# Kernel optimization log

Hardware: AMD Instinct MI355X
Metric: run time of the kernel (lower is better)

The kernel has to match this reference:

```python
import jax, jax.numpy as jnp
import numpy as np

B, C, RES, WS, HEADS, GROUPS, MLP_DIM = 16, 256, 56, 7, 8, 16, 1024
HEAD_DIM = C // HEADS
N = WS * WS  # tokens per window


def _rel_index(ws):
    coords = np.stack(np.meshgrid(np.arange(ws), np.arange(ws), indexing='ij'), 0).reshape(2, -1)
    rel = (coords[:, :, None] - coords[:, None, :]).transpose(1, 2, 0) + ws - 1
    return jnp.asarray(rel[..., 0] * (2 * ws - 1) + rel[..., 1], jnp.int32)


def setup_inputs() -> dict:
    key = jax.random.key(0)
    ks = jax.random.split(key, 8)
    s = 0.02
    return {
        'x': jax.random.normal(ks[0], (B, C, RES, RES), jnp.float32),
        'qkv_w': jax.random.normal(ks[1], (3 * C, C), jnp.float32) * s,
        'qkv_b': jnp.zeros((3 * C,), jnp.float32),
        'logit_scale': jnp.full((HEADS,), np.log(10.0), jnp.float32),
        'bias_table': jax.random.normal(ks[2], ((2 * WS - 1) ** 2, HEADS), jnp.float32) * s,
        'rel_index': _rel_index(WS),
        'proj_w': jax.random.normal(ks[3], (C, C), jnp.float32) * s,
        'proj_b': jnp.zeros((C,), jnp.float32),
        'gn1_w': jnp.ones((C,), jnp.float32), 'gn1_b': jnp.zeros((C,), jnp.float32),
        'gn2_w': jnp.ones((C,), jnp.float32), 'gn2_b': jnp.zeros((C,), jnp.float32),
        'mlp_gn_w': jnp.ones((C,), jnp.float32), 'mlp_gn_b': jnp.zeros((C,), jnp.float32),
        'mlp_w1': jax.random.normal(ks[4], (MLP_DIM, C), jnp.float32) * s,
        'mlp_b1': jnp.zeros((MLP_DIM,), jnp.float32),
        'mlp_w2': jax.random.normal(ks[5], (C, MLP_DIM), jnp.float32) * s,
        'mlp_b2': jnp.zeros((C,), jnp.float32),
    }


def _group_norm(x, w, b, groups, eps=1e-5):
    bn, c, h, ww = x.shape
    xg = x.reshape(bn, groups, c // groups, h, ww)
    m = xg.mean((2, 3, 4), keepdims=True)
    v = xg.var((2, 3, 4), keepdims=True)
    xg = (xg - m) * jax.lax.rsqrt(v + eps)
    return xg.reshape(bn, c, h, ww) * w[None, :, None, None] + b[None, :, None, None]


def _window_cosine_attn(x, qkv_w, qkv_b, logit_scale, bias_table, rel_index, proj_w, proj_b):
    bn, c, hh, ww = x.shape
    nh, nw = hh // WS, ww // WS
    # partition into non-overlapping WSxWS windows -> [bn*nh*nw, N, C]
    xw = x.reshape(bn, c, nh, WS, nw, WS).transpose(0, 2, 4, 3, 5, 1).reshape(bn * nh * nw, N, c)
    qkv = xw @ qkv_w.T + qkv_b
    qkv = qkv.reshape(-1, N, 3, HEADS, HEAD_DIM).transpose(2, 0, 3, 1, 4)
    q, k, v = qkv[0], qkv[1], qkv[2]  # [Bw, heads, N, d]
    # cosine attention (Swin v2): l2-normalized q/k, learnable clamped logit scale
    qn = q / jnp.clip(jnp.linalg.norm(q, axis=-1, keepdims=True), 1e-12)
    kn = k / jnp.clip(jnp.linalg.norm(k, axis=-1, keepdims=True), 1e-12)
    scale = jnp.exp(jnp.minimum(logit_scale, jnp.log(100.0)))[None, :, None, None]
    attn = jnp.einsum('bhnd,bhmd->bhnm', qn, kn) * scale
    bias = bias_table[rel_index].transpose(2, 0, 1)  # [heads, N, N]
    attn = jax.nn.softmax(attn + bias[None], axis=-1)
    out = jnp.einsum('bhnm,bhmd->bhnd', attn, v)
    out = out.transpose(0, 2, 1, 3).reshape(-1, N, c) @ proj_w.T + proj_b
    # reverse window partition -> [bn, c, H, W]
    out = out.reshape(bn, nh, nw, WS, WS, c).transpose(0, 5, 1, 3, 2, 4).reshape(bn, c, hh, ww)
    return out


def reference(x, qkv_w, qkv_b, logit_scale, bias_table, rel_index, proj_w, proj_b,
              gn1_w, gn1_b, gn2_w, gn2_b, mlp_gn_w, mlp_gn_b, mlp_w1, mlp_b1, mlp_w2, mlp_b2):
    h = _window_cosine_attn(x, qkv_w, qkv_b, logit_scale, bias_table, rel_index, proj_w, proj_b)
    h = jax.nn.relu(_group_norm(x + h, gn1_w, gn1_b, GROUPS))
    # ConvMLP: GroupNorm -> 1x1 conv -> act -> 1x1 conv
    m = _group_norm(h, mlp_gn_w, mlp_gn_b, GROUPS)
    m = jax.nn.relu(jnp.einsum('bchw,ec->behw', m, mlp_w1) + mlp_b1[None, :, None, None])
    m = jnp.einsum('behw,ce->bchw', m, mlp_w2) + mlp_b2[None, :, None, None]
    z = jax.nn.relu(_group_norm(h + m, gn2_w, gn2_b, GROUPS))
    return z
```

## Files before the change

kernel.cpp:

```cpp
#include <hip/hip_runtime.h>
#include <hip/hip_bf16.h>

typedef unsigned short u16;
typedef u16 u16x8 __attribute__((ext_vector_type(8)));
typedef u16 u16x4 __attribute__((ext_vector_type(4)));
typedef __bf16 bf16x8 __attribute__((ext_vector_type(8)));
typedef float f32x4 __attribute__((ext_vector_type(4)));

#define B_      16
#define C_      256
#define RES_    56
#define HW_     3136
#define NTOK    49
#define HEADS_  8
#define HD_     32
#define GROUPS_ 16
#define MLPD    1024
#define M_TOT   50176

__device__ __forceinline__ float b2f(u16 u){
  unsigned int x = ((unsigned int)u) << 16;
  return __builtin_bit_cast(float, x);
}
__device__ __forceinline__ u16 f2b(float f){
  __hip_bfloat16 h = __float2bfloat16(f);
  return __builtin_bit_cast(u16, h);
}
__device__ __forceinline__ bool sniff_f32(const void* sniff){
  return ((const u16*)sniff)[0] != (u16)0x3F80;
}
__device__ __forceinline__ float ldf(const void* p, size_t i, bool f32){
  return f32 ? ((const float*)p)[i] : b2f(((const u16*)p)[i]);
}
__device__ __forceinline__ void load8(const void* p, size_t off, bool f32, float* v){
  if (f32){
    const float* s = (const float*)p + off;
    float4 a = *(const float4*)s, b = *(const float4*)(s + 4);
    v[0]=a.x; v[1]=a.y; v[2]=a.z; v[3]=a.w; v[4]=b.x; v[5]=b.y; v[6]=b.z; v[7]=b.w;
  } else {
    u16x8 u = *(const u16x8*)((const u16*)p + off);
    #pragma unroll
    for (int j=0;j<8;++j) v[j] = b2f(u[j]);
  }
}

__device__ __forceinline__ void gload16(const u16* g, u16* l){
  __builtin_amdgcn_global_load_lds(
      (const __attribute__((address_space(1))) unsigned int*)g,
      (__attribute__((address_space(3))) unsigned int*)l, 16, 0, 0);
}

__device__ __forceinline__ int tok_of(int base_hw, int i){
  int ic = i < 48 ? i : 48;
  int q = (ic*37) >> 8;
  return base_hw + q*RES_ + (ic - q*7);
}

enum { M_QKV=0, M_PROJ=1, M_MLP1=2, M_MLP2=3 };

template<int MODE>
__global__ __launch_bounds__(256)
void mgemm(const u16* __restrict__ A, const u16* __restrict__ Bseg,
           const void* __restrict__ bias, void* __restrict__ Cp,
           const void* __restrict__ resid, float2* __restrict__ partE,
           const void* __restrict__ sniff)
{
  constexpr int KK  = (MODE==M_MLP2) ? 1024 : 256;
  constexpr bool STATS = (MODE==M_PROJ || MODE==M_MLP2);
  constexpr int BM  = STATS ? 64 : 128;
  constexpr int MFR = BM/32;
  const int nx  = gridDim.x;
  const int bid = blockIdx.y * nx + blockIdx.x;
  const int cpx = (nx * gridDim.y) >> 3;
  const int swz = (bid & 7) * cpx + (bid >> 3);
  const int n0 = (swz % nx) * 128;
  const int m0 = (swz / nx) * BM;

  __shared__ alignas(16) u16 As[BM*64];
  __shared__ alignas(16) u16 Bs[128*64];
  const int tid  = threadIdx.x;
  const int lane = tid & 63, w = tid >> 6;
  const int wm = w >> 1, wn = w & 1;
  const int lr = lane & 15, lk = lane >> 4;

  const int grow = lane >> 3, gcolg = (lane & 7) ^ (lane >> 3);
  size_t aoff[MFR], boff[4];
  #pragma unroll
  for (int i=0;i<MFR;++i){
    const int row = w*(BM/4) + i*8 + grow;
    aoff[i] = (size_t)(m0 + row)*KK + gcolg*8;
  }
  #pragma unroll
  for (int i=0;i<4;++i){
    const int row = w*32 + i*8 + grow;
    boff[i] = (size_t)(n0 + row)*KK + gcolg*8;
  }

  f32x4 acc[MFR][4];
  #pragma unroll
  for (int i=0;i<MFR;++i)
    #pragma unroll
    for (int j=0;j<4;++j) acc[i][j] = (f32x4){0.f,0.f,0.f,0.f};

  for (int k0 = 0; k0 < KK; k0 += 64){
    if (k0) __syncthreads();
    #pragma unroll
    for (int i=0;i<MFR;++i)
      gload16(A + aoff[i] + k0, As + (w*MFR+i)*512);
    #pragma unroll
    for (int i=0;i<4;++i)
      gload16(Bseg + boff[i] + k0, Bs + (w*4+i)*512);
    __syncthreads();
    #pragma unroll
    for (int kh=0; kh<2; ++kh){
      bf16x8 af[MFR], bfr[4];
      #pragma unroll
      for (int mf=0;mf<MFR;++mf){
        int row = wm*(BM/2) + mf*16 + lr;
        int idx = (row*64 + (kh*4 + lk)*8) ^ ((row&7)*8);
        af[mf] = *(const bf16x8*)(As + idx);
      }
      #pragma unroll
      for (int nf=0;nf<4;++nf){
        int row = wn*64 + nf*16 + lr;
        int idx = (row*64 + (kh*4 + lk)*8) ^ ((row&7)*8);
        bfr[nf] = *(const bf16x8*)(Bs + idx);
      }
      #pragma unroll
      for (int mf=0;mf<MFR;++mf)
        #pragma unroll
        for (int nf=0;nf<4;++nf)
          acc[mf][nf] = __builtin_amdgcn_mfma_f32_16x16x32_bf16(af[mf], bfr[nf], acc[mf][nf], 0,0,0);
    }
  }

  const bool f32 = sniff_f32(sniff);
  float bv[4];
  #pragma unroll
  for (int nf=0;nf<4;++nf)
    bv[nf] = ldf(bias, (size_t)(n0 + wn*64 + nf*16 + lr), f32);

  float sv[4] = {0.f,0.f,0.f,0.f};
  float qv[4] = {0.f,0.f,0.f,0.f};

  #pragma unroll
  for (int mf=0;mf<MFR;++mf){
    #pragma unroll
    for (int r=0;r<4;++r){
      const int row = m0 + wm*(BM/2) + mf*16 + lk*4 + r;
      #pragma unroll
      for (int nf=0;nf<4;++nf){
        const int col = n0 + wn*64 + nf*16 + lr;
        float v = acc[mf][nf][r] + bv[nf];
        if (MODE == M_QKV){
          ((u16*)Cp)[(size_t)row*768 + col] = f2b(v);
        } else if (MODE == M_MLP1){
          ((u16*)Cp)[(size_t)row*MLPD + col] = f2b(fmaxf(v, 0.f));
        } else {
          v += b2f(((const u16*)resid)[(size_t)row*C_ + col]);
          ((u16*)Cp)[(size_t)row*C_ + col] = f2b(v);
          if constexpr (STATS){ sv[nf] += v; qv[nf] += v*v; }
        }
      }
    }
  }

  if constexpr (STATS){
    const size_t tileId = (size_t)((m0>>6)*2 + (n0>>7));
    #pragma unroll
    for (int nf=0;nf<4;++nf){
      float s = sv[nf], q = qv[nf];
      #pragma unroll
      for (int m=1;m<64;m<<=1){ s += __shfl_xor(s,m); q += __shfl_xor(q,m); }
      if (lane == 0)
        partE[tileId*16 + w*4 + nf] = make_float2(s,q);
    }
  }
}

__global__ __launch_bounds__(256)
void xt_kernel(const void* __restrict__ x, u16* __restrict__ xbf,
               const void* __restrict__ sniff){
  const bool f32 = sniff_f32(sniff);
  const int hw0 = blockIdx.x*64, c0 = blockIdx.y*64, b = blockIdx.z;
  __shared__ float tile[64][65];
  const int t = threadIdx.x;
  {
    int r = t >> 2, p = t & 3;
    size_t src = ((size_t)(b*C_ + c0 + r))*HW_ + hw0 + p*16;
    float v[16];
    load8(x, src, f32, v);
    load8(x, src + 8, f32, v + 8);
    #pragma unroll
    for (int e=0;e<16;++e) tile[p*16+e][r] = v[e];
  }
  __syncthreads();
  {
    int r2 = t >> 2, p2 = t & 3;
    u16x8 o0, o1;
    #pragma unroll
    for (int e=0;e<8;++e){ o0[e] = f2b(tile[r2][p2*16+e]); o1[e] = f2b(tile[r2][p2*16+8+e]); }
    size_t dst = ((size_t)(b*HW_ + hw0 + r2))*C_ + c0 + p2*16;
    *(u16x8*)(xbf + dst)     = o0;
    *(u16x8*)(xbf + dst + 8) = o1;
  }
}

__global__ __launch_bounds__(256)
void wprep(const void* __restrict__ qkv_w, const void* __restrict__ proj_w,
           const void* __restrict__ w1, const void* __restrict__ w2,
           u16* __restrict__ wq, u16* __restrict__ wp,
           u16* __restrict__ w1b, u16* __restrict__ w2b,
           const void* __restrict__ bias_table, const int* __restrict__ rel_index,
           float* __restrict__ biasD, float* __restrict__ biasRM,
           const void* __restrict__ sniff){
  const bool f32 = sniff_f32(sniff);
  const int blk = blockIdx.x;
  if (blk < 384){
    const void* src; u16* dst; int base;
    if (blk < 96)      { src = qkv_w;  dst = wq;  base = blk; }
    else if (blk <128) { src = proj_w; dst = wp;  base = blk - 96; }
    else if (blk <256) { src = w1;     dst = w1b; base = blk - 128; }
    else               { src = w2;     dst = w2b; base = blk - 256; }
    int i = (base*256 + threadIdx.x)*8;
    float v[8];
    load8(src, (size_t)i, f32, v);
    u16x8 u;
    #pragma unroll
    for (int j=0;j<8;++j) u[j] = f2b(v[j]);
    *(u16x8*)(dst + i) = u;
  } else {
    int h = blk - 384;
    for (int idx = threadIdx.x; idx < NTOK*NTOK; idx += 256)
      biasD[h*NTOK*NTOK + idx] = ldf(bias_table, (size_t)rel_index[idx]*HEADS_ + h, f32);
    __syncthreads();
    for (int i = threadIdx.x; i < NTOK; i += 256){
      const float* row = biasD + (h*NTOK + i)*NTOK;
      float m = row[0];
      for (int j=1;j<NTOK;++j) m = fmaxf(m, row[j]);
      biasRM[h*NTOK + i] = m;
    }
  }
}

__global__ __launch_bounds__(256)
void attn_kernel(const u16* __restrict__ qkv, u16* __restrict__ attnout,
                 const void* __restrict__ logit_scale, const float* __restrict__ biasD,
                 const float* __restrict__ biasRM, const void* __restrict__ sniff)
{
  const bool f32 = sniff_f32(sniff);
  const int h = blockIdx.x & 7, w = blockIdx.x >> 3;
  const int b = w >> 6, wr = (w >> 3) & 7, wc = w & 7;
  const int tid = threadIdx.x;
  const int wv = tid >> 6, lane = tid & 63;
  const int lr = lane & 15, lg = lane >> 4;
  const int base_hw = (wr*7)*RES_ + wc*7;
  const size_t qbase = (size_t)b*HW_*768;

  __shared__ alignas(16) u16 Qn[64][40];
  __shared__ alignas(16) u16 Kn[64][40];
  __shared__ alignas(16) u16 Vt[32][72];
  __shared__ alignas(16) u16 Pl[64][72];

  const float scale = __expf(fminf(ldf(logit_scale, h, f32), 4.6051701860f));

  if (wv == 0){
    u16 vrow[32];
    if (lane < NTOK){
      const u16* src = qkv + qbase + (size_t)tok_of(base_hw, lane)*768 + 512 + h*HD_;
      u16x8 a0 = *(const u16x8*)(src), a1 = *(const u16x8*)(src+8);
      u16x8 a2 = *(const u16x8*)(src+16), a3 = *(const u16x8*)(src+24);
      #pragma unroll
      for (int e=0;e<8;++e){ vrow[e]=a0[e]; vrow[8+e]=a1[e]; vrow[16+e]=a2[e]; vrow[24+e]=a3[e]; }
    } else {
      #pragma unroll
      for (int e=0;e<32;++e) vrow[e] = 0;
    }
    #pragma unroll
    for (int d=0;d<32;++d) Vt[d][lane] = vrow[d];
  } else if (wv == 1 || wv == 2){
    float fv[32];
    if (lane < NTOK){
      const u16* src = qkv + qbase + (size_t)tok_of(base_hw, lane)*768
                     + (wv == 2 ? 0 : 256) + h*HD_;
      #pragma unroll
      for (int c8=0;c8<4;++c8){
        u16x8 u = *(const u16x8*)(src + c8*8);
        #pragma unroll
        for (int e=0;e<8;++e) fv[c8*8+e] = b2f(u[e]);
      }
    } else {
      #pragma unroll
      for (int e=0;e<32;++e) fv[e] = 0.f;
    }
    float ss = 0.f;
    #pragma unroll
    for (int d=0;d<32;++d) ss += fv[d]*fv[d];
    float inv = (wv == 2 ? scale : 1.f) / fmaxf(sqrtf(ss), 1e-12f);
    u16* dst = (wv == 2) ? &Qn[lane][0] : &Kn[lane][0];
    #pragma unroll
    for (int c8=0;c8<4;++c8){
      u16x8 u;
      #pragma unroll
      for (int e=0;e<8;++e) u[e] = f2b(fv[c8*8+e]*inv);
      *(u16x8*)(dst + c8*8) = u;
    }
  }
  __syncthreads();

  const int mt = wv;
  const int i0 = mt*16;

  bf16x8 af = *(const bf16x8*)&Qn[i0 + lr][lg*8];
  f32x4 s[4];
  #pragma unroll
  for (int nt=0;nt<4;++nt){
    bf16x8 bq = *(const bf16x8*)&Kn[nt*16 + lr][lg*8];
    f32x4 c;
    #pragma unroll
    for (int r=0;r<4;++r){
      int i = i0 + lg*4 + r; if (i > 48) i = 48;
      int j = nt*16 + lr;    if (j > 48) j = 48;
      c[r] = biasD[((size_t)h*NTOK + i)*NTOK + j];
    }
    s[nt] = __builtin_amdgcn_mfma_f32_16x16x32_bf16(af, bq, c, 0,0,0);
  }

  float isum[4];
  #pragma unroll
  for (int r=0;r<4;++r){
    const int i = i0 + lg*4 + r;
    const int ic = i > 48 ? 48 : i;
    const float m = scale + biasRM[h*NTOK + ic];
    float ps = 0.f;
    #pragma unroll
    for (int nt=0;nt<4;++nt){
      const int j = nt*16 + lr;
      float p = (j < NTOK) ? __expf(s[nt][r] - m) : 0.f;
      Pl[i][j] = f2b(p);
      ps += p;
    }
    ps += __shfl_xor(ps,1); ps += __shfl_xor(ps,2);
    ps += __shfl_xor(ps,4); ps += __shfl_xor(ps,8);
    isum[r] = 1.f / ps;
  }

  f32x4 o[2];
  o[0] = (f32x4){0.f,0.f,0.f,0.f};
  o[1] = (f32x4){0.f,0.f,0.f,0.f};
  #pragma unroll
  for (int kk=0;kk<2;++kk){
    bf16x8 pa = *(const bf16x8*)&Pl[i0 + lr][kk*32 + lg*8];
    #pragma unroll
    for (int nt=0;nt<2;++nt){
      bf16x8 pb = *(const bf16x8*)&Vt[nt*16 + lr][kk*32 + lg*8];
      o[nt] = __builtin_amdgcn_mfma_f32_16x16x32_bf16(pa, pb, o[nt], 0,0,0);
    }
  }

  #pragma unroll
  for (int r=0;r<4;++r){
    const int i = i0 + lg*4 + r;
    if (i < NTOK){
      size_t ob = ((size_t)(b*HW_) + tok_of(base_hw, i))*C_ + h*HD_;
      attnout[ob + lr]      = f2b(o[0][r] * isum[r]);
      attnout[ob + 16 + lr] = f2b(o[1][r] * isum[r]);
    }
  }
}

__global__ __launch_bounds__(256)
void statsE_fin(const float2* __restrict__ partE, float2* __restrict__ AB,
                const void* __restrict__ w, const void* __restrict__ bb,
                const void* __restrict__ sniff){
  const int b = blockIdx.x, t = threadIdx.x;
  const int g = t & 15, ch = t >> 4;
  const int ntI = g >> 3, wn_ = (g >> 2) & 1, nf = g & 3;
  float s = 0.f, q = 0.f;
  int i0 = ch*4, i1 = i0 + 4 > 49 ? 49 : i0 + 4;
  for (int i = i0; i < i1; ++i){
    size_t base = ((size_t)((b*49 + i)*2 + ntI))*16;
    float2 p0 = partE[base + wn_*4 + nf];
    float2 p1 = partE[base + 8 + wn_*4 + nf];
    s += p0.x + p1.x; q += p0.y + p1.y;
  }
  __shared__ float Ls[256], Lq[256];
  Ls[t] = s; Lq[t] = q;
  __syncthreads();
  if (t < 16){
    float ss = 0.f, qq = 0.f;
    #pragma unroll
    for (int c=0;c<16;++c){ ss += Ls[c*16 + t]; qq += Lq[c*16 + t]; }
    float mean = ss * (1.f/50176.f);
    float var  = fmaxf(qq * (1.f/50176.f) - mean*mean, 0.f);
    float rsig = rsqrtf(var + 1e-5f);
    const bool f32 = sniff_f32(sniff);
    for (int e=0;e<16;++e){
      int k = t*16 + e;
      float a = rsig * ldf(w, k, f32);
      AB[b*256 + k] = make_float2(a, ldf(bb, k, f32) - mean*a);
    }
  }
}

__global__ __launch_bounds__(256)
void stats_fin2(const float2* __restrict__ part2, float2* __restrict__ AB,
                const void* __restrict__ w, const void* __restrict__ bb,
                const void* __restrict__ sniff){
  const int b = blockIdx.x, t = threadIdx.x;
  const int g = t & 15, ch = t >> 4;
  float s = 0.f, q = 0.f;
  int i0 = ch*25, i1 = i0 + 25 > 392 ? 392 : i0 + 25;
  for (int i = i0; i < i1; ++i){
    float2 p = part2[(size_t)(b*392 + i)*16 + g];
    s += p.x; q += p.y;
  }
  __shared__ float Ls[256], Lq[256];
  Ls[t] = s; Lq[t] = q;
  __syncthreads();
  if (t < 16){
    float ss = 0.f, qq = 0.f;
    #pragma unroll
    for (int c=0;c<16;++c){ ss += Ls[c*16 + t]; qq += Lq[c*16 + t]; }
    float mean = ss * (1.f/50176.f);
    float var  = fmaxf(qq * (1.f/50176.f) - mean*mean, 0.f);
    float rsig = rsqrtf(var + 1e-5f);
    const bool f32 = sniff_f32(sniff);
    for (int e=0;e<16;++e){
      int k = t*16 + e;
      float a = rsig * ldf(w, k, f32);
      AB[b*256 + k] = make_float2(a, ldf(bb, k, f32) - mean*a);
    }
  }
}

__global__ __launch_bounds__(256)
void gnrelu_kernel(const u16* __restrict__ Yb, const float2* __restrict__ AB1,
                   float2* __restrict__ part2, u16* __restrict__ Hb){
  size_t base = (size_t)blockIdx.x * 2048;
  int b = blockIdx.x / 392;
  int t = threadIdx.x;
  int off = t * 8;
  int c0 = off & 255;
  u16x8 uin = *(const u16x8*)(Yb + base + off);
  u16x8 u; float s=0.f, q=0.f;
  #pragma unroll
  for (int j=0;j<8;++j){
    float2 ab = AB1[b*256 + c0 + j];
    float o = fmaxf(b2f(uin[j])*ab.x + ab.y, 0.f);
    u[j] = f2b(o);
    s += o; q += o*o;
  }
  *(u16x8*)(Hb + base + off) = u;
  __shared__ float Ls[256], Lq[256];
  Ls[t] = s; Lq[t] = q;
  __syncthreads();
  if (t < 16){
    float ss=0.f, qq=0.f;
    #pragma unroll
    for (int j=0;j<16;++j){
      int idx = t*2 + (j&1) + (j>>1)*32;
      ss += Ls[idx]; qq += Lq[idx];
    }
    part2[(size_t)blockIdx.x*16 + t] = make_float2(ss,qq);
  }
}

__global__ __launch_bounds__(256)
void hnorm_kernel(const u16* __restrict__ Hb, const float2* __restrict__ AB,
                  u16* __restrict__ Hn){
  size_t base = (size_t)blockIdx.x * 2048;
  int b = blockIdx.x / 392;
  int off = threadIdx.x * 8;
  int c0 = off & 255;
  u16x8 uin = *(const u16x8*)(Hb + base + off);
  u16x8 u;
  #pragma unroll
  for (int j=0;j<8;++j){
    float2 ab = AB[b*256 + c0 + j];
    u[j] = f2b(b2f(uin[j])*ab.x + ab.y);
  }
  *(u16x8*)(Hn + base + off) = u;
}

__global__ __launch_bounds__(256)
void out_kernel(const u16* __restrict__ T, const float2* __restrict__ AB2,
                void* __restrict__ outp, const void* __restrict__ sniff){
  const bool f32 = sniff_f32(sniff);
  int hw0 = blockIdx.x*64, c0 = blockIdx.y*64, b = blockIdx.z;
  __shared__ float tile[64][68];
  {
    int r = threadIdx.x >> 2, p = threadIdx.x & 3;
    const u16* src = T + ((size_t)(b*HW_ + hw0 + r))*C_ + c0 + p*16;
    u16x8 v0 = *(const u16x8*)(src);
    u16x8 v1 = *(const u16x8*)(src + 8);
    #pragma unroll
    for (int e=0;e<16;++e){
      int cl = p*16 + e;
      int c = c0 + cl;
      float2 ab = AB2[b*256 + c];
      float tv = b2f(e < 8 ? v0[e] : v1[e-8]);
      tile[cl][r] = fmaxf(tv*ab.x + ab.y, 0.f);
    }
  }
  __syncthreads();
  {
    int r2 = threadIdx.x >> 2, p2 = threadIdx.x & 3;
    size_t ob = ((size_t)(b*C_ + c0 + r2))*HW_ + hw0 + p2*16;
    if (f32){
      float* op = (float*)outp;
      #pragma unroll
      for (int q4=0;q4<4;++q4){
        float4 vv = *(const float4*)&tile[r2][p2*16 + q4*4];
        *(float4*)(op + ob + q4*4) = vv;
      }
    } else {
      u16* op = (u16*)outp;
      u16x8 u0, u1;
      #pragma unroll
      for (int e=0;e<8;++e) u0[e] = f2b(tile[r2][p2*16 + e]);
      #pragma unroll
      for (int e=0;e<8;++e) u1[e] = f2b(tile[r2][p2*16 + 8 + e]);
      *(u16x8*)(op + ob)     = u0;
      *(u16x8*)(op + ob + 8) = u1;
    }
  }
}

__global__ void marker_kernel(u16* o){ o[threadIdx.x] = 0x4640; }

extern "C" void kernel_launch(void* const* d_in, const int* in_sizes, int n_in,
                              void* d_out, int out_size, void* d_ws, size_t ws_size,
                              hipStream_t stream)
{
  const void* x           = d_in[0];
  const void* qkv_w       = d_in[1];
  const void* qkv_b       = d_in[2];
  const void* logit_scale = d_in[3];
  const void* bias_table  = d_in[4];
  const int*  rel_index   = (const int*)d_in[5];
  const void* proj_w      = d_in[6];
  const void* proj_b      = d_in[7];
  const void* gn1_w       = d_in[8];
  const void* gn1_b       = d_in[9];
  const void* gn2_w       = d_in[10];
  const void* gn2_b       = d_in[11];
  const void* mgn_w       = d_in[12];
  const void* mgn_b       = d_in[13];
  const void* w1          = d_in[14];
  const void* b1          = d_in[15];
  const void* w2          = d_in[16];
  const void* b2          = d_in[17];

  char* ws = (char*)d_ws;
  const size_t o_qkv  = 0ull;
  const size_t o_attn = 77070336ull;
  const size_t o_Y    = 102760448ull;
  const size_t o_H    = 154140672ull;
  const size_t o_wbf  = 205527040ull;
  const size_t o_bd   = 207099904ull;
  const size_t o_brm  = 207176736ull;
  const size_t o_ab   = 207178304ull;
  const size_t o_ab1  = 207227456ull;
  const size_t o_ab2  = 207260224ull;
  const size_t o_p2   = 207292992ull;
  const size_t need   = 208095808ull;
  if (ws_size < need){
    marker_kernel<<<1, 256, 0, stream>>>((u16*)d_out);
    return;
  }

  u16*   qkvbuf  = (u16*)(ws + o_qkv);
  u16*   attnbuf = (u16*)(ws + o_attn);
  u16*   Yb      = (u16*)(ws + o_Y);
  u16*   Hb      = (u16*)(ws + o_H);
  u16*   xbf     = (u16*)(ws + o_H);
  u16*   Hn      = (u16*)(ws + o_Y);
  u16*   M1      = (u16*)(ws + o_qkv);
  u16*   T       = (u16*)(ws + o_Y);
  u16*   wq      = (u16*)(ws + o_wbf);
  u16*   wp      = wq + 768*256;
  u16*   w1b     = wp + 256*256;
  u16*   w2b     = w1b + 1024*256;
  float* biasD   = (float*)(ws + o_bd);
  float* biasRM  = (float*)(ws + o_brm);
  float2* ABm    = (float2*)(ws + o_ab);
  float2* AB1    = (float2*)(ws + o_ab1);
  float2* AB2    = (float2*)(ws + o_ab2);
  float2* part2  = (float2*)(ws + o_p2);
  float2* partE  = (float2*)(ws + o_p2);
  const void* sniff = gn1_w;

  wprep        <<<392, 256, 0, stream>>>(qkv_w, proj_w, w1, w2, wq, wp, w1b, w2b,
                                         bias_table, rel_index, biasD, biasRM, sniff);
  xt_kernel    <<<dim3(49,4,16), 256, 0, stream>>>(x, xbf, sniff);

  mgemm<M_QKV ><<<dim3(6,392), 256, 0, stream>>>(xbf, wq, qkv_b, qkvbuf, nullptr, nullptr, sniff);
  attn_kernel  <<<8192, 256, 0, stream>>>(qkvbuf, attnbuf, logit_scale, biasD, biasRM, sniff);
  mgemm<M_PROJ><<<dim3(2,784), 256, 0, stream>>>(attnbuf, wp, proj_b, Yb, xbf, partE, sniff);
  statsE_fin   <<<16, 256, 0, stream>>>(partE, AB1, gn1_w, gn1_b, sniff);
  gnrelu_kernel<<<6272, 256, 0, stream>>>(Yb, AB1, part2, Hb);
  stats_fin2   <<<16, 256, 0, stream>>>(part2, ABm, mgn_w, mgn_b, sniff);
  hnorm_kernel <<<6272, 256, 0, stream>>>(Hb, ABm, Hn);
  mgemm<M_MLP1><<<dim3(8,392), 256, 0, stream>>>(Hn, w1b, b1, M1, nullptr, nullptr, sniff);
  mgemm<M_MLP2><<<dim3(2,784), 256, 0, stream>>>(M1, w2b, b2, T, Hb, partE, sniff);
  statsE_fin   <<<16, 256, 0, stream>>>(partE, AB2, gn2_w, gn2_b, sniff);
  out_kernel   <<<dim3(49,4,16), 256, 0, stream>>>(T, AB2, d_out, sniff);
}
```

Before: 261.7 us.

## Fold MLP GroupNorm affine into per-batch W1 and bias, drop hnorm pass

The per-batch GroupNorm scale/shift before the first MLP 1x1 conv is folded into a per-batch copy of W1 (columns scaled) and a per-batch bias, so the hnorm elementwise pass over the activation tensor is removed and MLP1 reads the un-normalized H directly. All GEMMs now use a 64-row M tile, which doubles the QKV and MLP1 grids. This saves a full read and write of the H tensor but adds 16 per-batch weight copies (8 MB) that MLP1 must stream. Smaller tiles also lower arithmetic intensity. Scaling the weights in bf16 changes rounding slightly.

```diff
diff --git a/kernel.cpp b/kernel.cpp
--- a/kernel.cpp
+++ b/kernel.cpp
@@ -67,16 +67,15 @@
 {
   constexpr int KK  = (MODE==M_MLP2) ? 1024 : 256;
   constexpr bool STATS = (MODE==M_PROJ || MODE==M_MLP2);
-  constexpr int BM  = STATS ? 64 : 128;
-  constexpr int MFR = BM/32;
   const int nx  = gridDim.x;
   const int bid = blockIdx.y * nx + blockIdx.x;
   const int cpx = (nx * gridDim.y) >> 3;
   const int swz = (bid & 7) * cpx + (bid >> 3);
   const int n0 = (swz % nx) * 128;
-  const int m0 = (swz / nx) * BM;
-
-  __shared__ alignas(16) u16 As[BM*64];
+  const int m0 = (swz / nx) * 64;
+  const int bt = m0 / HW_;
+
+  __shared__ alignas(16) u16 As[64*64];
   __shared__ alignas(16) u16 Bs[128*64];
   const int tid  = threadIdx.x;
   const int lane = tid & 63, w = tid >> 6;
@@ -84,39 +83,40 @@
   const int lr = lane & 15, lk = lane >> 4;
 
   const int grow = lane >> 3, gcolg = (lane & 7) ^ (lane >> 3);
-  size_t aoff[MFR], boff[4];
-  #pragma unroll
-  for (int i=0;i<MFR;++i){
-    const int row = w*(BM/4) + i*8 + grow;
+  size_t aoff[2], boff[4];
+  #pragma unroll
+  for (int i=0;i<2;++i){
+    const int row = w*16 + i*8 + grow;
     aoff[i] = (size_t)(m0 + row)*KK + gcolg*8;
   }
+  const size_t bbase = (MODE==M_MLP1) ? (size_t)bt*MLPD*KK : 0;
   #pragma unroll
   for (int i=0;i<4;++i){
     const int row = w*32 + i*8 + grow;
-    boff[i] = (size_t)(n0 + row)*KK + gcolg*8;
-  }
-
-  f32x4 acc[MFR][4];
-  #pragma unroll
-  for (int i=0;i<MFR;++i)
+    boff[i] = bbase + (size_t)(n0 + row)*KK + gcolg*8;
+  }
+
+  f32x4 acc[2][4];
+  #pragma unroll
+  for (int i=0;i<2;++i)
     #pragma unroll
     for (int j=0;j<4;++j) acc[i][j] = (f32x4){0.f,0.f,0.f,0.f};
 
   for (int k0 = 0; k0 < KK; k0 += 64){
     if (k0) __syncthreads();
     #pragma unroll
-    for (int i=0;i<MFR;++i)
-      gload16(A + aoff[i] + k0, As + (w*MFR+i)*512);
+    for (int i=0;i<2;++i)
+      gload16(A + aoff[i] + k0, As + (w*2+i)*512);
     #pragma unroll
     for (int i=0;i<4;++i)
       gload16(Bseg + boff[i] + k0, Bs + (w*4+i)*512);
     __syncthreads();
     #pragma unroll
     for (int kh=0; kh<2; ++kh){
-      bf16x8 af[MFR], bfr[4];
-      #pragma unroll
-      for (int mf=0;mf<MFR;++mf){
-        int row = wm*(BM/2) + mf*16 + lr;
+      bf16x8 af[2], bfr[4];
+      #pragma unroll
+      for (int mf=0;mf<2;++mf){
+        int row = wm*32 + mf*16 + lr;
         int idx = (row*64 + (kh*4 + lk)*8) ^ ((row&7)*8);
         af[mf] = *(const bf16x8*)(As + idx);
       }
@@ -127,7 +127,7 @@
         bfr[nf] = *(const bf16x8*)(Bs + idx);
       }
       #pragma unroll
-      for (int mf=0;mf<MFR;++mf)
+      for (int mf=0;mf<2;++mf)
         #pragma unroll
         for (int nf=0;nf<4;++nf)
           acc[mf][nf] = __builtin_amdgcn_mfma_f32_16x16x32_bf16(af[mf], bfr[nf], acc[mf][nf], 0,0,0);
@@ -137,17 +137,20 @@
   const bool f32 = sniff_f32(sniff);
   float bv[4];
   #pragma unroll
-  for (int nf=0;nf<4;++nf)
-    bv[nf] = ldf(bias, (size_t)(n0 + wn*64 + nf*16 + lr), f32);
+  for (int nf=0;nf<4;++nf){
+    const size_t ci = (size_t)(n0 + wn*64 + nf*16 + lr);
+    bv[nf] = (MODE==M_MLP1) ? ((const float*)bias)[(size_t)bt*MLPD + ci]
+                            : ldf(bias, ci, f32);
+  }
 
   float sv[4] = {0.f,0.f,0.f,0.f};
   float qv[4] = {0.f,0.f,0.f,0.f};
 
   #pragma unroll
-  for (int mf=0;mf<MFR;++mf){
+  for (int mf=0;mf<2;++mf){
     #pragma unroll
     for (int r=0;r<4;++r){
-      const int row = m0 + wm*(BM/2) + mf*16 + lk*4 + r;
+      const int row = m0 + wm*32 + mf*16 + lk*4 + r;
       #pragma unroll
       for (int nf=0;nf<4;++nf){
         const int col = n0 + wn*64 + nf*16 + lr;
@@ -244,6 +247,36 @@
 }
 
 __global__ __launch_bounds__(256)
+void w1mod_pre(const u16* __restrict__ w1b, const void* __restrict__ b1,
+               const float2* __restrict__ ABm, u16* __restrict__ w1mod,
+               float* __restrict__ b1mod, const void* __restrict__ sniff){
+  const bool f32 = sniff_f32(sniff);
+  const int b = blockIdx.x >> 5, eg = blockIdx.x & 31;
+  const int t = threadIdx.x;
+  const int e = eg*32 + (t >> 3);
+  const int c0 = (t & 7) * 32;
+  float partial = 0.f;
+  #pragma unroll
+  for (int q=0;q<4;++q){
+    u16x8 wv = *(const u16x8*)(w1b + (size_t)e*C_ + c0 + q*8);
+    u16x8 o;
+    #pragma unroll
+    for (int j=0;j<8;++j){
+      float2 ab = ABm[b*C_ + c0 + q*8 + j];
+      float wf = b2f(wv[j]);
+      o[j] = f2b(wf * ab.x);
+      partial += wf * ab.y;
+    }
+    *(u16x8*)(w1mod + ((size_t)b*MLPD + e)*C_ + c0 + q*8) = o;
+  }
+  partial += __shfl_xor(partial, 1);
+  partial += __shfl_xor(partial, 2);
+  partial += __shfl_xor(partial, 4);
+  if ((t & 7) == 0)
+    b1mod[b*MLPD + e] = ldf(b1, e, f32) + partial;
+}
+
+__global__ __launch_bounds__(256)
 void attn_kernel(const u16* __restrict__ qkv, u16* __restrict__ attnout,
                  const void* __restrict__ logit_scale, const float* __restrict__ biasD,
                  const float* __restrict__ biasRM, const void* __restrict__ sniff)
@@ -464,23 +497,6 @@
     }
     part2[(size_t)blockIdx.x*16 + t] = make_float2(ss,qq);
   }
-}
-
-__global__ __launch_bounds__(256)
-void hnorm_kernel(const u16* __restrict__ Hb, const float2* __restrict__ AB,
-                  u16* __restrict__ Hn){
-  size_t base = (size_t)blockIdx.x * 2048;
-  int b = blockIdx.x / 392;
-  int off = threadIdx.x * 8;
-  int c0 = off & 255;
-  u16x8 uin = *(const u16x8*)(Hb + base + off);
-  u16x8 u;
-  #pragma unroll
-  for (int j=0;j<8;++j){
-    float2 ab = AB[b*256 + c0 + j];
-    u[j] = f2b(b2f(uin[j])*ab.x + ab.y);
-  }
-  *(u16x8*)(Hn + base + off) = u;
 }
 
 __global__ __launch_bounds__(256)
@@ -564,7 +580,9 @@
   const size_t o_ab1  = 207227456ull;
   const size_t o_ab2  = 207260224ull;
   const size_t o_p2   = 207292992ull;
-  const size_t need   = 208095808ull;
+  const size_t o_w1m  = 208095808ull;
+  const size_t o_b1m  = 216484416ull;
+  const size_t need   = 216549952ull;
   if (ws_size < need){
     marker_kernel<<<1, 256, 0, stream>>>((u16*)d_out);
     return;
@@ -575,7 +593,6 @@
   u16*   Yb      = (u16*)(ws + o_Y);
   u16*   Hb      = (u16*)(ws + o_H);
   u16*   xbf     = (u16*)(ws + o_H);
-  u16*   Hn      = (u16*)(ws + o_Y);
   u16*   M1      = (u16*)(ws + o_qkv);
   u16*   T       = (u16*)(ws + o_Y);
   u16*   wq      = (u16*)(ws + o_wbf);
@@ -589,20 +606,22 @@
   float2* AB2    = (float2*)(ws + o_ab2);
   float2* part2  = (float2*)(ws + o_p2);
   float2* partE  = (float2*)(ws + o_p2);
+  u16*   w1mod   = (u16*)(ws + o_w1m);
+  float* b1mod   = (float*)(ws + o_b1m);
   const void* sniff = gn1_w;
 
   wprep        <<<392, 256, 0, stream>>>(qkv_w, proj_w, w1, w2, wq, wp, w1b, w2b,
                                          bias_table, rel_index, biasD, biasRM, sniff);
   xt_kernel    <<<dim3(49,4,16), 256, 0, stream>>>(x, xbf, sniff);
 
-  mgemm<M_QKV ><<<dim3(6,392), 256, 0, stream>>>(xbf, wq, qkv_b, qkvbuf, nullptr, nullptr, sniff);
+  mgemm<M_QKV ><<<dim3(6,784), 256, 0, stream>>>(xbf, wq, qkv_b, qkvbuf, nullptr, nullptr, sniff);
   attn_kernel  <<<8192, 256, 0, stream>>>(qkvbuf, attnbuf, logit_scale, biasD, biasRM, sniff);
   mgemm<M_PROJ><<<dim3(2,784), 256, 0, stream>>>(attnbuf, wp, proj_b, Yb, xbf, partE, sniff);
   statsE_fin   <<<16, 256, 0, stream>>>(partE, AB1, gn1_w, gn1_b, sniff);
   gnrelu_kernel<<<6272, 256, 0, stream>>>(Yb, AB1, part2, Hb);
   stats_fin2   <<<16, 256, 0, stream>>>(part2, ABm, mgn_w, mgn_b, sniff);
-  hnorm_kernel <<<6272, 256, 0, stream>>>(Hb, ABm, Hn);
-  mgemm<M_MLP1><<<dim3(8,392), 256, 0, stream>>>(Hn, w1b, b1, M1, nullptr, nullptr, sniff);
+  w1mod_pre    <<<512, 256, 0, stream>>>(w1b, b1, ABm, w1mod, b1mod, sniff);
+  mgemm<M_MLP1><<<dim3(8,784), 256, 0, stream>>>(Hb, w1mod, b1mod, M1, nullptr, nullptr, sniff);
   mgemm<M_MLP2><<<dim3(2,784), 256, 0, stream>>>(M1, w2b, b2, T, Hb, partE, sniff);
   statsE_fin   <<<16, 256, 0, stream>>>(partE, AB2, gn2_w, gn2_b, sniff);
   out_kernel   <<<dim3(49,4,16), 256, 0, stream>>>(T, AB2, d_out, sniff);
```

Measured after the change: 271.2 us. +3.6%, slower.
